# Optimization experiments

Measured on AMD Instinct MI355X. Metric: run time of the kernel, lower is better.

Reference implementation:

```python
import jax, jax.numpy as jnp
import numpy as np

IN, OUT, STEPS, BATCH = 1024, 1024, 100, 64
THR = 15.0
RATIO = 0.5
C1 = RATIO * THR            # initial membrane potential = 7.5
C2 = 1.0 / THR
C3 = (1.0 - RATIO) / STEPS


def setup_inputs() -> dict:
    key = jax.random.key(0)
    k0, k1, k2, k3 = jax.random.split(key, 4)
    spikes = jax.random.randint(k0, (STEPS, BATCH, IN), 0, 2).astype(jnp.float32)
    mem = jnp.full((BATCH, OUT), C1, dtype=jnp.float32)          # init_if
    hat_spikes = jax.random.uniform(k1, (BATCH, IN), dtype=jnp.float32)
    W = jax.random.normal(k2, (OUT, IN), dtype=jnp.float32)      # w_mean=0, w_std=1
    b = jax.random.normal(k3, (OUT,), dtype=jnp.float32)
    return {"spikes": spikes, "mem": mem, "hat_spikes": hat_spikes, "W": W, "b": b}


def reference(spikes, mem, hat_spikes, W, b):
    steps = spikes.shape[0]
    # delta_us = fc(spikes): [T, B, OUT]
    delta_us = jnp.einsum('tbi,oi->tbo', spikes, W) + b

    def step(carry, du):
        m, su = carry
        m = m + du
        s = (m > THR).astype(m.dtype)          # spike
        m = jnp.clip(m, 0.0, THR)              # clamp_(0, thr)
        su = su + m                            # sum_u += mem
        m = m - m * s                          # reset fired neurons
        return (m, su), s

    (mem_out, sum_u), ss = jax.lax.scan(
        step, (mem, jnp.zeros_like(mem)), delta_us)

    hat_u_fwd = sum_u / steps                  # [B, OUT]
    hat_s_fwd = ss.mean(axis=0)                # [B, OUT]

    # training-mode surrogate path: forward values come from the spike loop,
    # gradients flow through fc(hat_spikes) (ForwardFirstBackwardSecond)
    delta_u = hat_spikes @ W.T + b
    hat_u = jax.lax.stop_gradient(hat_u_fwd) + delta_u - jax.lax.stop_gradient(delta_u)
    surr = jnp.maximum(hat_u * C2, C3)         # (hat_u*C2).clamp_min(C3)
    hat_s = jax.lax.stop_gradient(hat_s_fwd) + surr - jax.lax.stop_gradient(surr)

    return ss, mem_out, hat_s
```

## Files before the change

kernel.cpp:

```cpp
#include <hip/hip_runtime.h>


typedef __attribute__((ext_vector_type(4))) int int4v;

#define T_STEPS 100
#define T_PAD   112
#define BO      65536
#define K_DIM   1024
#define A8_OFF  0
#define BT_OFF  7340032
#define LDS_BUF 23552

__global__ __launch_bounds__(256)
void prepass(const float* __restrict__ S, const float* __restrict__ W,
             signed char* __restrict__ A8, signed char* __restrict__ Bt) {
    const int wave = blockIdx.x * 4 + (threadIdx.x >> 6);
    const int lane = threadIdx.x & 63;
    const int r16 = lane & 15, quad = lane >> 4;

    if (wave < 7168) {
        const int b   = wave / 112;
        const int rem = wave - b * 112;
        const int jt  = rem >> 4, k64 = rem & 15;
        const int t   = jt * 16 + r16;
        union { signed char c[16]; int4v v; } u;
        if (t < T_STEPS) {
            const float* sp = S + ((size_t)t * 64 + b) * K_DIM + k64 * 64 + quad * 16;
            const float4 s0 = *(const float4*)(sp);
            const float4 s1 = *(const float4*)(sp + 4);
            const float4 s2 = *(const float4*)(sp + 8);
            const float4 s3 = *(const float4*)(sp + 12);
            const float sv[16] = {s0.x,s0.y,s0.z,s0.w, s1.x,s1.y,s1.z,s1.w,
                                  s2.x,s2.y,s2.z,s2.w, s3.x,s3.y,s3.z,s3.w};
#pragma unroll
            for (int e = 0; e < 16; ++e) u.c[e] = (signed char)sv[e];
        } else {
#pragma unroll
            for (int e = 0; e < 16; ++e) u.c[e] = 0;
        }
        *(int4v*)(A8 + (size_t)wave * 1024 + lane * 16) = u.v;
    } else {
        const int t2 = wave - 7168;
        const int n16 = t2 >> 4, k64 = t2 & 15;
        const int n = n16 * 16 + r16;
        const float* wp = W + (size_t)n * K_DIM + k64 * 64 + quad * 16;
        const float4 w0 = *(const float4*)(wp);
        const float4 w1 = *(const float4*)(wp + 4);
        const float4 w2 = *(const float4*)(wp + 8);
        const float4 w3 = *(const float4*)(wp + 12);
        const float wv[16] = {w0.x,w0.y,w0.z,w0.w, w1.x,w1.y,w1.z,w1.w,
                              w2.x,w2.y,w2.z,w2.w, w3.x,w3.y,w3.z,w3.w};
        union { signed char c[16]; int4v v; } u[4];
#pragma unroll
        for (int e = 0; e < 16; ++e) {
            long long q = llrint((double)wv[e] * 0x1p28);
#pragma unroll
            for (int p = 0; p < 3; ++p) {
                const int d = (int)(((q + 128) & 255) - 128);
                u[p].c[e] = (signed char)d;
                q = (q - d) >> 8;
            }
            u[3].c[e] = (signed char)q;
        }
        signed char* base = Bt + (size_t)(n16 * 16 + k64) * 4 * 1024 + lane * 16;
#pragma unroll
        for (int p = 0; p < 4; ++p)
            *(int4v*)(base + (size_t)p * 1024) = u[p].v;
    }
}

__global__ __launch_bounds__(256, 2)
void gemm_scan(const signed char* __restrict__ A8,
               const signed char* __restrict__ Bt,
               const float* __restrict__ bias,
               const float* __restrict__ mem0,
               float* __restrict__ out) {
    __shared__ int4v lds4[3200];
    signed char* slds = (signed char*)lds4;
    double* dulds = (double*)lds4;

    const int bid = blockIdx.x;
    const int b  = bid >> 4;
    const int ng = bid & 15;

    const int tid = threadIdx.x;
    const int lane = tid & 63, wid = tid >> 6;
    const int quad = lane >> 4, r16 = lane & 15;

    const signed char* sbase[6];
    int sstride[6], ldsoff[6];
#pragma unroll
    for (int j = 0; j < 6; ++j) {
        const int c = wid + 4 * j;
        const int cc = (c < 23) ? c : 0;
        if (cc < 7) {
            sbase[j] = A8 + ((size_t)(b * T_PAD + cc * 16)) * 1024 + lane * 16;
            sstride[j] = 1024;
            ldsoff[j] = cc * 1024 + lane * 16;
        } else {
            const int j2 = cc - 7;
            sbase[j] = Bt + ((size_t)((ng * 4 + (j2 >> 2)) * 16) * 4 + (j2 & 3)) * 1024
                          + lane * 16;
            sstride[j] = 4096;
            ldsoff[j] = 7168 + j2 * 1024 + lane * 16;
        }
    }
    int aoff[7], boff[4];
#pragma unroll
    for (int i = 0; i < 7; ++i) aoff[i] = i * 1024 + lane * 16;
#pragma unroll
    for (int p = 0; p < 4; ++p) boff[p] = 7168 + (wid * 4 + p) * 1024 + lane * 16;

    int4v sreg[6];
    int4v acc[7][4] = {};

#pragma unroll
    for (int j = 0; j < 6; ++j) if (wid + 4 * j < 23) sreg[j] = *(const int4v*)(sbase[j]);
#pragma unroll
    for (int j = 0; j < 6; ++j) if (wid + 4 * j < 23) *(int4v*)(slds + ldsoff[j]) = sreg[j];
    __syncthreads();

    for (int kt = 0; kt < 16; ++kt) {
        const int cur = (kt & 1) * LDS_BUF, nxt = LDS_BUF - cur;
        if (kt + 1 < 16) {
#pragma unroll
            for (int j = 0; j < 6; ++j) if (wid + 4 * j < 23)
                sreg[j] = *(const int4v*)(sbase[j] + (size_t)(kt + 1) * sstride[j]);
        }
        int4v af[7], bf[4];
#pragma unroll
        for (int i = 0; i < 7; ++i) af[i] = *(const int4v*)(slds + cur + aoff[i]);
#pragma unroll
        for (int p = 0; p < 4; ++p) bf[p] = *(const int4v*)(slds + cur + boff[p]);
#pragma unroll
        for (int p = 0; p < 4; ++p)
#pragma unroll
            for (int i = 0; i < 7; ++i)
                acc[i][p] = __builtin_amdgcn_mfma_i32_16x16x64_i8(
                    af[i], bf[p], acc[i][p], 0, 0, 0);
        if (kt + 1 < 16) {
#pragma unroll
            for (int j = 0; j < 6; ++j) if (wid + 4 * j < 23)
                *(int4v*)(slds + nxt + ldsoff[j]) = sreg[j];
        }
        __syncthreads();
    }

    const int n_loc = wid * 16 + r16;
    const double bd = (double)bias[ng * 64 + n_loc];
#pragma unroll
    for (int i = 0; i < 7; ++i)
#pragma unroll
        for (int e = 0; e < 4; ++e) {
            const int t = i * 16 + quad * 4 + e;
            if (t < T_STEPS) {
                long long v = (long long)acc[i][3][e];
                v = v * 256 + (long long)acc[i][2][e];
                v = v * 256 + (long long)acc[i][1][e];
                v = v * 256 + (long long)acc[i][0][e];
                dulds[t * 64 + n_loc] = (double)v * 0x1p-28 + bd;
            }
        }
    __syncthreads();

    if (wid == 0) {
        const int bo = b * 1024 + ng * 64 + lane;
        double m = (double)mem0[bo];
        double cnt = 0.0;
        double d[4];
#pragma unroll
        for (int u = 0; u < 4; ++u) d[u] = dulds[u * 64 + lane];
        for (int g = 0; g < 25; ++g) {
            double dn[4];
            if (g + 1 < 25) {
#pragma unroll
                for (int u = 0; u < 4; ++u) dn[u] = dulds[((g + 1) * 4 + u) * 64 + lane];
            }
#pragma unroll
            for (int u = 0; u < 4; ++u) {
                m += d[u];
                const double s = (m > 15.0) ? 1.0 : 0.0;
                m = fmin(fmax(m, 0.0), 15.0);
                out[(size_t)(g * 4 + u) * BO + bo] = (float)s;
                cnt += s;
                m -= m * s;
            }
            if (g + 1 < 25) {
#pragma unroll
                for (int u = 0; u < 4; ++u) d[u] = dn[u];
            }
        }
        out[(size_t)T_STEPS * BO + bo] = (float)m;
        out[(size_t)(T_STEPS + 1) * BO + bo] = (float)(cnt * 0.01);
    }
}

extern "C" void kernel_launch(void* const* d_in, const int* in_sizes, int n_in,
                              void* d_out, int out_size, void* d_ws, size_t ws_size,
                              hipStream_t stream) {
    const float* spikes = (const float*)d_in[0];
    const float* mem    = (const float*)d_in[1];
    const float* W      = (const float*)d_in[3];
    const float* b      = (const float*)d_in[4];
    float* out = (float*)d_out;
    signed char* A8 = (signed char*)d_ws + A8_OFF;
    signed char* Bt = (signed char*)d_ws + BT_OFF;

    prepass<<<dim3(2048), 256, 0, stream>>>(spikes, W, A8, Bt);
    gemm_scan<<<dim3(1024), 256, 0, stream>>>(A8, Bt, b, mem, out);
}
```

Baseline: 126.6 us.

## Replace LDS-staged 4-wave GEMM blocks with single-wave blocks reading fragments directly

The GEMM+scan kernel now launches 4096 single-wave blocks, each owning one batch row and 16 output neurons. Each wave loads its A and B MFMA fragments straight from global memory instead of staging them through a double-buffered LDS tile with barriers. The scan is now run by 16 lanes per block, so four times as many blocks run the serial loop in parallel. The cost is that each A tile is no longer shared across four waves and is re-fetched by more blocks, which raises global and L2 traffic, and each scan block uses only a quarter of its wave.

```diff
diff --git a/kernel.cpp b/kernel.cpp
--- a/kernel.cpp
+++ b/kernel.cpp
@@ -9,7 +9,6 @@
 #define K_DIM   1024
 #define A8_OFF  0
 #define BT_OFF  7340032
-#define LDS_BUF 23552
 
 __global__ __launch_bounds__(256)
 void prepass(const float* __restrict__ S, const float* __restrict__ W,
@@ -69,85 +68,43 @@
     }
 }
 
-__global__ __launch_bounds__(256, 2)
+__global__ __launch_bounds__(64, 3)
 void gemm_scan(const signed char* __restrict__ A8,
                const signed char* __restrict__ Bt,
                const float* __restrict__ bias,
                const float* __restrict__ mem0,
                float* __restrict__ out) {
-    __shared__ int4v lds4[3200];
-    signed char* slds = (signed char*)lds4;
-    double* dulds = (double*)lds4;
+    __shared__ double dulds[T_STEPS * 16];
 
     const int bid = blockIdx.x;
-    const int b  = bid >> 4;
-    const int ng = bid & 15;
+    const int ng  = bid >> 6;
+    const int b   = bid & 63;
 
-    const int tid = threadIdx.x;
-    const int lane = tid & 63, wid = tid >> 6;
+    const int lane = threadIdx.x & 63;
     const int quad = lane >> 4, r16 = lane & 15;
 
-    const signed char* sbase[6];
-    int sstride[6], ldsoff[6];
-#pragma unroll
-    for (int j = 0; j < 6; ++j) {
-        const int c = wid + 4 * j;
-        const int cc = (c < 23) ? c : 0;
-        if (cc < 7) {
-            sbase[j] = A8 + ((size_t)(b * T_PAD + cc * 16)) * 1024 + lane * 16;
-            sstride[j] = 1024;
-            ldsoff[j] = cc * 1024 + lane * 16;
-        } else {
-            const int j2 = cc - 7;
-            sbase[j] = Bt + ((size_t)((ng * 4 + (j2 >> 2)) * 16) * 4 + (j2 & 3)) * 1024
-                          + lane * 16;
-            sstride[j] = 4096;
-            ldsoff[j] = 7168 + j2 * 1024 + lane * 16;
-        }
-    }
-    int aoff[7], boff[4];
-#pragma unroll
-    for (int i = 0; i < 7; ++i) aoff[i] = i * 1024 + lane * 16;
-#pragma unroll
-    for (int p = 0; p < 4; ++p) boff[p] = 7168 + (wid * 4 + p) * 1024 + lane * 16;
+    const signed char* abase = A8 + (size_t)b * T_PAD * 1024 + lane * 16;
+    const signed char* bbase = Bt + (size_t)ng * 65536 + lane * 16;
 
-    int4v sreg[6];
     int4v acc[7][4] = {};
 
-#pragma unroll
-    for (int j = 0; j < 6; ++j) if (wid + 4 * j < 23) sreg[j] = *(const int4v*)(sbase[j]);
-#pragma unroll
-    for (int j = 0; j < 6; ++j) if (wid + 4 * j < 23) *(int4v*)(slds + ldsoff[j]) = sreg[j];
-    __syncthreads();
-
     for (int kt = 0; kt < 16; ++kt) {
-        const int cur = (kt & 1) * LDS_BUF, nxt = LDS_BUF - cur;
-        if (kt + 1 < 16) {
-#pragma unroll
-            for (int j = 0; j < 6; ++j) if (wid + 4 * j < 23)
-                sreg[j] = *(const int4v*)(sbase[j] + (size_t)(kt + 1) * sstride[j]);
-        }
         int4v af[7], bf[4];
 #pragma unroll
-        for (int i = 0; i < 7; ++i) af[i] = *(const int4v*)(slds + cur + aoff[i]);
+        for (int i = 0; i < 7; ++i)
+            af[i] = *(const int4v*)(abase + (size_t)(i * 16 + kt) * 1024);
 #pragma unroll
-        for (int p = 0; p < 4; ++p) bf[p] = *(const int4v*)(slds + cur + boff[p]);
+        for (int p = 0; p < 4; ++p)
+            bf[p] = *(const int4v*)(bbase + (size_t)(kt * 4 + p) * 1024);
 #pragma unroll
         for (int p = 0; p < 4; ++p)
 #pragma unroll
             for (int i = 0; i < 7; ++i)
                 acc[i][p] = __builtin_amdgcn_mfma_i32_16x16x64_i8(
                     af[i], bf[p], acc[i][p], 0, 0, 0);
-        if (kt + 1 < 16) {
-#pragma unroll
-            for (int j = 0; j < 6; ++j) if (wid + 4 * j < 23)
-                *(int4v*)(slds + nxt + ldsoff[j]) = sreg[j];
-        }
-        __syncthreads();
     }
 
-    const int n_loc = wid * 16 + r16;
-    const double bd = (double)bias[ng * 64 + n_loc];
+    const double bd = (double)bias[ng * 16 + r16];
 #pragma unroll
     for (int i = 0; i < 7; ++i)
 #pragma unroll
@@ -158,23 +115,23 @@
                 v = v * 256 + (long long)acc[i][2][e];
                 v = v * 256 + (long long)acc[i][1][e];
                 v = v * 256 + (long long)acc[i][0][e];
-                dulds[t * 64 + n_loc] = (double)v * 0x1p-28 + bd;
+                dulds[t * 16 + r16] = (double)v * 0x1p-28 + bd;
             }
         }
     __syncthreads();
 
-    if (wid == 0) {
-        const int bo = b * 1024 + ng * 64 + lane;
+    if (lane < 16) {
+        const int bo = b * 1024 + ng * 16 + lane;
         double m = (double)mem0[bo];
         double cnt = 0.0;
         double d[4];
 #pragma unroll
-        for (int u = 0; u < 4; ++u) d[u] = dulds[u * 64 + lane];
+        for (int u = 0; u < 4; ++u) d[u] = dulds[u * 16 + lane];
         for (int g = 0; g < 25; ++g) {
             double dn[4];
             if (g + 1 < 25) {
 #pragma unroll
-                for (int u = 0; u < 4; ++u) dn[u] = dulds[((g + 1) * 4 + u) * 64 + lane];
+                for (int u = 0; u < 4; ++u) dn[u] = dulds[((g + 1) * 4 + u) * 16 + lane];
             }
 #pragma unroll
             for (int u = 0; u < 4; ++u) {
@@ -207,5 +164,5 @@
     signed char* Bt = (signed char*)d_ws + BT_OFF;
 
     prepass<<<dim3(2048), 256, 0, stream>>>(spikes, W, A8, Bt);
-    gemm_scan<<<dim3(1024), 256, 0, stream>>>(A8, Bt, b, mem, out);
+    gemm_scan<<<dim3(4096), 64, 0, stream>>>(A8, Bt, b, mem, out);
 }
```

Result: slower. 219.8 us (+73.6%).
